# Kernel tuning notes

Hardware: AMD Instinct MI355X
Metric: run time of the kernel (lower is better)

## Reference

```python
import jax, jax.numpy as jnp
import numpy as np
import math

B, L, C, H = 8, 1024, 1024, 8
EPS = 1e-5

def setup_inputs() -> dict:
    key = jax.random.key(0)
    ks = jax.random.split(key, 5)
    s = 0.02
    return {
        "x": jax.random.normal(ks[0], (B, L, C), dtype=jnp.float32),
        "ln_g": jnp.ones((C,), dtype=jnp.float32),
        "ln_b": jnp.zeros((C,), dtype=jnp.float32),
        "w_qkv": jax.random.normal(ks[1], (C, 3 * C), dtype=jnp.float32) * s,
        "b_qkv": jax.random.normal(ks[2], (3 * C,), dtype=jnp.float32) * s,
        "w_out": jax.random.normal(ks[3], (C, C), dtype=jnp.float32) * s,
        "b_out": jax.random.normal(ks[4], (C,), dtype=jnp.float32) * s,
    }

def reference(x, ln_g, ln_b, w_qkv, b_qkv, w_out, b_out):
    bs, length, width = x.shape
    ch = width // H
    # LayerNorm over channels
    mu = jnp.mean(x, axis=-1, keepdims=True)
    var = jnp.mean(jnp.square(x - mu), axis=-1, keepdims=True)
    xn = (x - mu) * jax.lax.rsqrt(var + EPS) * ln_g + ln_b
    # fused QKV projection
    qkv = jnp.einsum('blc,cd->bld', xn, w_qkv) + b_qkv  # [B, L, 3C]
    q, k, v = jnp.split(qkv, 3, axis=2)                 # each [B, L, C]
    scale = 1.0 / math.sqrt(math.sqrt(ch))
    # faithful raw row-major reshape as in the torch .view call
    q = (q * scale).reshape(bs * H, length, ch)
    k = (k * scale).reshape(bs * H, length, ch)
    v = v.reshape(bs * H, length, ch)
    w = jnp.einsum('bqc,bkc->bqk', q, k)                # [B*H, L, L] score matrix
    w = jax.nn.softmax(w.astype(jnp.float32), axis=-1).astype(q.dtype)
    attn = jnp.einsum('bqk,bkc->bqc', w, v).reshape(bs, length, -1)
    out = jnp.einsum('blc,cd->bld', attn, w_out) + b_out + xn  # residual uses normalized x
    return out
```

## Files before the change

kernel.cpp:

```cpp
#include <hip/hip_runtime.h>
#include <hip/hip_bf16.h>


typedef __attribute__((ext_vector_type(8))) short short8;
typedef __attribute__((ext_vector_type(4))) float f32x4;

#define QK_SCALE 0.29730177875068026f

__device__ __forceinline__ float bf2f(ushort u) {
    union { float f; unsigned int i; } c; c.i = ((unsigned int)u) << 16; return c.f;
}
__device__ __forceinline__ ushort f2bf(float f) {
    union { float f; unsigned int i; } c; c.f = f;
    unsigned int x = c.i;
    return (ushort)((x + 0x7FFFu + ((x >> 16) & 1u)) >> 16);
}

__device__ __forceinline__ void gload_lds16(const ushort* g, ushort* l) {
    __builtin_amdgcn_global_load_lds(
        (const __attribute__((address_space(1))) unsigned int*)g,
        (__attribute__((address_space(3))) unsigned int*)l, 16, 0, 0);
}

__global__ __launch_bounds__(256) void ln_kernel(
    const float* __restrict__ x, const float* __restrict__ g,
    const float* __restrict__ b, ushort* __restrict__ xn) {
    int row = blockIdx.x;
    int tid = threadIdx.x;
    const float* xr = x + (size_t)row * 1024;
    float4 v4 = *(const float4*)(xr + tid * 4);
    float v[4] = {v4.x, v4.y, v4.z, v4.w};
    float s1 = 0.f, s2 = 0.f;
#pragma unroll
    for (int j = 0; j < 4; j++) { s1 += v[j]; s2 += v[j] * v[j]; }
#pragma unroll
    for (int m = 32; m >= 1; m >>= 1) { s1 += __shfl_xor(s1, m); s2 += __shfl_xor(s2, m); }
    __shared__ float r1[4], r2[4];
    int lane = tid & 63, w = tid >> 6;
    if (lane == 0) { r1[w] = s1; r2[w] = s2; }
    __syncthreads();
    s1 = r1[0] + r1[1] + r1[2] + r1[3];
    s2 = r2[0] + r2[1] + r2[2] + r2[3];
    float mu = s1 * (1.0f / 1024.0f);
    float var = s2 * (1.0f / 1024.0f) - mu * mu;
    float rs = rsqrtf(var + 1e-5f);
    int c0 = tid * 4;
    float4 gg = *(const float4*)(g + c0);
    float4 bb = *(const float4*)(b + c0);
    float gA[4] = {gg.x, gg.y, gg.z, gg.w};
    float bA[4] = {bb.x, bb.y, bb.z, bb.w};
    ushort o[4];
#pragma unroll
    for (int j = 0; j < 4; j++) o[j] = f2bf((v[j] - mu) * rs * gA[j] + bA[j]);
    uint2 pk;
    pk.x = (uint)o[0] | ((uint)o[1] << 16);
    pk.y = (uint)o[2] | ((uint)o[3] << 16);
    *(uint2*)(xn + (size_t)row * 1024 + c0) = pk;
}

__global__ __launch_bounds__(256) void transpose_kernel(
    const float* __restrict__ in, ushort* __restrict__ out, int R, int Cc) {
    __shared__ ushort t[32][33];
    int bx = blockIdx.x * 32, by = blockIdx.y * 32;
    int tx = threadIdx.x & 31, ty = threadIdx.x >> 5;
#pragma unroll
    for (int j = 0; j < 32; j += 8)
        t[ty + j][tx] = f2bf(in[(size_t)(by + ty + j) * Cc + bx + tx]);
    __syncthreads();
#pragma unroll
    for (int j = 0; j < 32; j += 8)
        out[(size_t)(bx + ty + j) * R + by + tx] = t[tx][ty + j];
}

__global__ __launch_bounds__(256) void transpose_head(
    const ushort* __restrict__ in, ushort* __restrict__ out) {
    __shared__ ushort t[32][33];
    int h = blockIdx.z;
    int j0 = blockIdx.y * 32;
    int d0 = blockIdx.x * 32;
    int tx = threadIdx.x & 31, ty = threadIdx.x >> 5;
    const ushort* src = in + (size_t)h * 131072;
    ushort* dst = out + (size_t)h * 131072;
#pragma unroll
    for (int j = 0; j < 32; j += 8)
        t[ty + j][tx] = src[(size_t)(j0 + ty + j) * 128 + d0 + tx];
    __syncthreads();
#pragma unroll
    for (int j = 0; j < 32; j += 8)
        dst[(size_t)(d0 + ty + j) * 1024 + j0 + tx] = t[tx][ty + j];
}

__global__ __launch_bounds__(256) void gemm_qkv(
    const ushort* __restrict__ A, const ushort* __restrict__ Bt,
    const float* __restrict__ bias, ushort* __restrict__ out0,
    ushort* __restrict__ out1, ushort* __restrict__ out2) {
    const int K = 1024;
    __shared__ __align__(16) ushort As[128 * 64];
    __shared__ __align__(16) ushort Bs[128 * 64];

    int tid = threadIdx.x;
    int lane = tid & 63, w = tid >> 6;
    int l15 = lane & 15, q4 = lane >> 4;
    int wr = (w >> 1) * 64, wc = (w & 1) * 64;
    int rowBase = blockIdx.y * 128, colBase = blockIdx.x * 128;

    f32x4 acc[4][4];
    f32x4 zero = {0.f, 0.f, 0.f, 0.f};
#pragma unroll
    for (int mi = 0; mi < 4; mi++)
#pragma unroll
        for (int ni = 0; ni < 4; ni++) acc[mi][ni] = zero;

    for (int kt = 0; kt < 16; kt++) {
        __syncthreads();
#pragma unroll
        for (int i = 0; i < 4; i++) {
            int linear = i * 256 + w * 64 + lane;
            int r = linear >> 3, p = linear & 7;
            int l = p ^ (r & 7);
            gload_lds16(&A[(size_t)(rowBase + r) * K + kt * 64 + l * 8], &As[linear * 8]);
            gload_lds16(&Bt[(size_t)(colBase + r) * K + kt * 64 + l * 8], &Bs[linear * 8]);
        }
        __syncthreads();

#pragma unroll
        for (int kk = 0; kk < 2; kk++) {
            short8 aF[4], bF[4];
#pragma unroll
            for (int mi = 0; mi < 4; mi++) {
                int r = wr + mi * 16 + l15;
                aF[mi] = *(const short8*)&As[r * 64 + ((kk * 4 + q4) ^ (r & 7)) * 8];
            }
#pragma unroll
            for (int ni = 0; ni < 4; ni++) {
                int r = wc + ni * 16 + l15;
                bF[ni] = *(const short8*)&Bs[r * 64 + ((kk * 4 + q4) ^ (r & 7)) * 8];
            }
#pragma unroll
            for (int mi = 0; mi < 4; mi++)
#pragma unroll
                for (int ni = 0; ni < 4; ni++)
                    acc[mi][ni] = __builtin_amdgcn_mfma_f32_16x16x32_bf16(
                        aF[mi], bF[ni], acc[mi][ni], 0, 0, 0);
        }
    }

#pragma unroll
    for (int mi = 0; mi < 4; mi++)
#pragma unroll
        for (int ni = 0; ni < 4; ni++) {
            f32x4 a = acc[mi][ni];
            int col = colBase + wc + ni * 16 + l15;
            float bv = bias[col];
#pragma unroll
            for (int r = 0; r < 4; r++) {
                int row = rowBase + wr + mi * 16 + q4 * 4 + r;
                float val = a[r] + bv;
                if (col < 2048) val *= QK_SCALE;
                int bsel = col >> 10, cc = col & 1023;
                ushort* dst = (bsel == 0) ? out0 : ((bsel == 1) ? out1 : out2);
                dst[(size_t)row * 1024 + cc] = f2bf(val);
            }
        }
}

__global__ __launch_bounds__(256, 4) void gemm_out(
    const ushort* __restrict__ A, const ushort* __restrict__ Bt,
    const float* __restrict__ bias, const ushort* __restrict__ resid,
    float* __restrict__ outf) {
    const int K = 1024;
    __shared__ __align__(16) ushort As[64 * 64];
    __shared__ __align__(16) ushort Bs[128 * 64];

    int tid = threadIdx.x;
    int lane = tid & 63, w = tid >> 6;
    int l15 = lane & 15, q4 = lane >> 4;
    int wr = (w >> 1) * 32, wc = (w & 1) * 64;
    int rowBase = blockIdx.y * 64, colBase = blockIdx.x * 128;

    f32x4 acc[2][4];
    f32x4 zero = {0.f, 0.f, 0.f, 0.f};
#pragma unroll
    for (int mi = 0; mi < 2; mi++)
#pragma unroll
        for (int ni = 0; ni < 4; ni++) acc[mi][ni] = zero;

    for (int kt = 0; kt < 16; kt++) {
        __syncthreads();
#pragma unroll
        for (int i = 0; i < 6; i++) {
            int id = i * 256 + w * 64 + lane;
            if (id < 512) {
                int r = id >> 3, p = id & 7;
                int l = p ^ (r & 7);
                gload_lds16(&A[(size_t)(rowBase + r) * K + kt * 64 + l * 8], &As[id * 8]);
            } else {
                int idb = id - 512;
                int r = idb >> 3, p = idb & 7;
                int l = p ^ (r & 7);
                gload_lds16(&Bt[(size_t)(colBase + r) * K + kt * 64 + l * 8], &Bs[idb * 8]);
            }
        }
        __syncthreads();

#pragma unroll
        for (int kk = 0; kk < 2; kk++) {
            short8 aF[2], bF[4];
#pragma unroll
            for (int mi = 0; mi < 2; mi++) {
                int r = wr + mi * 16 + l15;
                aF[mi] = *(const short8*)&As[r * 64 + ((kk * 4 + q4) ^ (r & 7)) * 8];
            }
#pragma unroll
            for (int ni = 0; ni < 4; ni++) {
                int r = wc + ni * 16 + l15;
                bF[ni] = *(const short8*)&Bs[r * 64 + ((kk * 4 + q4) ^ (r & 7)) * 8];
            }
#pragma unroll
            for (int mi = 0; mi < 2; mi++)
#pragma unroll
                for (int ni = 0; ni < 4; ni++)
                    acc[mi][ni] = __builtin_amdgcn_mfma_f32_16x16x32_bf16(
                        aF[mi], bF[ni], acc[mi][ni], 0, 0, 0);
        }
    }

#pragma unroll
    for (int mi = 0; mi < 2; mi++)
#pragma unroll
        for (int ni = 0; ni < 4; ni++) {
            f32x4 a = acc[mi][ni];
            int col = colBase + wc + ni * 16 + l15;
            float bv = bias[col];
#pragma unroll
            for (int r = 0; r < 4; r++) {
                int row = rowBase + wr + mi * 16 + q4 * 4 + r;
                float val = a[r] + bv + bf2f(resid[(size_t)row * 1024 + col]);
                outf[(size_t)row * 1024 + col] = val;
            }
        }
}

__global__ __launch_bounds__(256, 4) void attn_kernel(
    const ushort* __restrict__ qb, const ushort* __restrict__ kb,
    const ushort* __restrict__ vt, ushort* __restrict__ ob) {
    int g = blockIdx.x >> 4;
    int qblk = blockIdx.x & 15;
    const ushort* Qh = qb + (size_t)g * 131072;
    const ushort* Kh = kb + (size_t)g * 131072;
    const ushort* Vh = vt + (size_t)g * 131072;

    __shared__ __align__(16) ushort Ks[64 * 128];
    __shared__ __align__(16) ushort Vt[128 * 64];
    __shared__ __align__(16) ushort Ps[64 * 64];

    int tid = threadIdx.x, lane = tid & 63, w = tid >> 6;
    int l15 = lane & 15, q4 = lane >> 4;
    int q0 = qblk * 64;

    short8 qf[4];
#pragma unroll
    for (int ks = 0; ks < 4; ks++)
        qf[ks] = *(const short8*)&Qh[(size_t)(q0 + w * 16 + l15) * 128 + ks * 32 + q4 * 8];

    f32x4 zero = {0.f, 0.f, 0.f, 0.f};
    f32x4 o[8];
#pragma unroll
    for (int ni = 0; ni < 8; ni++) o[ni] = zero;
    float plsum[4] = {0.f, 0.f, 0.f, 0.f};

    for (int kt = 0; kt < 16; kt++) {
        __syncthreads();
#pragma unroll
        for (int i = 0; i < 4; i++) {
            int linear = i * 256 + w * 64 + lane;
            int r = linear >> 4, p = linear & 15;
            int l = p ^ (r & 15);
            gload_lds16(&Kh[(size_t)(kt * 64 + r) * 128 + l * 8], &Ks[linear * 8]);
        }
#pragma unroll
        for (int i = 0; i < 4; i++) {
            int id = i * 256 + tid;
            int d = id >> 3, c = id & 7;
            int pc = c ^ (d & 7);
            *(uint4*)&Vt[d * 64 + pc * 8] =
                *(const uint4*)&Vh[(size_t)d * 1024 + kt * 64 + c * 8];
        }
        __syncthreads();

        f32x4 sacc[4];
#pragma unroll
        for (int ni = 0; ni < 4; ni++) sacc[ni] = zero;
#pragma unroll
        for (int ks = 0; ks < 4; ks++) {
#pragma unroll
            for (int ni = 0; ni < 4; ni++) {
                int r = ni * 16 + l15;
                int p = (ks * 4 + q4) ^ (r & 15);
                short8 bF = *(const short8*)&Ks[r * 128 + p * 8];
                sacc[ni] = __builtin_amdgcn_mfma_f32_16x16x32_bf16(
                    qf[ks], bF, sacc[ni], 0, 0, 0);
            }
        }

#pragma unroll
        for (int ni = 0; ni < 4; ni++) {
#pragma unroll
            for (int r = 0; r < 4; r++) {
                float pv = __expf(sacc[ni][r]);
                plsum[r] += pv;
                int qloc = w * 16 + q4 * 4 + r;
                int key = ni * 16 + l15;
                int pc = (key >> 3) ^ (qloc & 7);
                Ps[qloc * 64 + pc * 8 + (key & 7)] = f2bf(pv);
            }
        }

#pragma unroll
        for (int ks2 = 0; ks2 < 2; ks2++) {
            int c = ks2 * 4 + q4;
            short8 aF = *(const short8*)&Ps[(w * 16 + l15) * 64 + (c ^ (l15 & 7)) * 8];
#pragma unroll
            for (int ni = 0; ni < 8; ni++) {
                int d = ni * 16 + l15;
                short8 bF = *(const short8*)&Vt[d * 64 + (c ^ (d & 7)) * 8];
                o[ni] = __builtin_amdgcn_mfma_f32_16x16x32_bf16(aF, bF, o[ni], 0, 0, 0);
            }
        }
    }

#pragma unroll
    for (int r = 0; r < 4; r++) {
#pragma unroll
        for (int m = 1; m < 16; m <<= 1) plsum[r] += __shfl_xor(plsum[r], m, 16);
    }
    float inv[4];
#pragma unroll
    for (int r = 0; r < 4; r++) inv[r] = 1.0f / plsum[r];
#pragma unroll
    for (int ni = 0; ni < 8; ni++)
#pragma unroll
        for (int r = 0; r < 4; r++) {
            int qrow = q0 + w * 16 + q4 * 4 + r;
            ob[(size_t)g * 131072 + (size_t)qrow * 128 + ni * 16 + l15] =
                f2bf(o[ni][r] * inv[r]);
        }
}

extern "C" void kernel_launch(void* const* d_in, const int* in_sizes, int n_in,
                              void* d_out, int out_size, void* d_ws, size_t ws_size,
                              hipStream_t stream) {
    const float* x     = (const float*)d_in[0];
    const float* ln_g  = (const float*)d_in[1];
    const float* ln_b  = (const float*)d_in[2];
    const float* w_qkv = (const float*)d_in[3];
    const float* b_qkv = (const float*)d_in[4];
    const float* w_out = (const float*)d_in[5];
    const float* b_out = (const float*)d_in[6];
    float* out = (float*)d_out;

    const size_t MC = 8192ull * 1024ull;
    ushort* xn    = (ushort*)d_ws;
    ushort* wqkvT = xn + MC;
    ushort* woutT = wqkvT + 3072ull * 1024ull;
    ushort* qbuf  = woutT + 1024ull * 1024ull;
    ushort* kbuf  = qbuf + MC;
    ushort* vtbuf = kbuf + MC;
    ushort* attnb = vtbuf + MC;

    ln_kernel<<<8192, 256, 0, stream>>>(x, ln_g, ln_b, xn);
    transpose_kernel<<<dim3(96, 32), 256, 0, stream>>>(w_qkv, wqkvT, 1024, 3072);
    transpose_kernel<<<dim3(32, 32), 256, 0, stream>>>(w_out, woutT, 1024, 1024);
    gemm_qkv<<<dim3(24, 64), 256, 0, stream>>>(xn, wqkvT, b_qkv, qbuf, kbuf, attnb);
    transpose_head<<<dim3(4, 32, 64), 256, 0, stream>>>(attnb, vtbuf);
    attn_kernel<<<1024, 256, 0, stream>>>(qbuf, kbuf, vtbuf, attnb);
    gemm_out<<<dim3(8, 128), 256, 0, stream>>>(attnb, woutT, b_out, xn, out);
}
```

Before: 268.4 us.

## Merge prep kernels and write transposed V directly from QKV GEMM epilogue

LayerNorm and both weight transposes are merged into one prep kernel, with LayerNorm now handling one row per wavefront. The QKV GEMM epilogue writes V straight into the per-head transposed layout, so the separate transpose_head kernel and its extra round trip through global memory are gone. GEMM load addresses are precomputed and advanced by pointer increments rather than recomputed every k-step. The cost is strided, uncoalesced 2-byte stores in the V epilogue.

```diff
diff --git a/kernel.cpp b/kernel.cpp
--- a/kernel.cpp
+++ b/kernel.cpp
@@ -22,78 +22,73 @@
         (__attribute__((address_space(3))) unsigned int*)l, 16, 0, 0);
 }
 
-__global__ __launch_bounds__(256) void ln_kernel(
+__global__ __launch_bounds__(256) void prep_kernel(
     const float* __restrict__ x, const float* __restrict__ g,
-    const float* __restrict__ b, ushort* __restrict__ xn) {
-    int row = blockIdx.x;
+    const float* __restrict__ b, ushort* __restrict__ xn,
+    const float* __restrict__ w_qkv, ushort* __restrict__ wqkvT,
+    const float* __restrict__ w_out, ushort* __restrict__ woutT) {
+    __shared__ ushort t[32][33];
+    int bid = blockIdx.x;
     int tid = threadIdx.x;
-    const float* xr = x + (size_t)row * 1024;
-    float4 v4 = *(const float4*)(xr + tid * 4);
-    float v[4] = {v4.x, v4.y, v4.z, v4.w};
-    float s1 = 0.f, s2 = 0.f;
-#pragma unroll
-    for (int j = 0; j < 4; j++) { s1 += v[j]; s2 += v[j] * v[j]; }
-#pragma unroll
-    for (int m = 32; m >= 1; m >>= 1) { s1 += __shfl_xor(s1, m); s2 += __shfl_xor(s2, m); }
-    __shared__ float r1[4], r2[4];
-    int lane = tid & 63, w = tid >> 6;
-    if (lane == 0) { r1[w] = s1; r2[w] = s2; }
-    __syncthreads();
-    s1 = r1[0] + r1[1] + r1[2] + r1[3];
-    s2 = r2[0] + r2[1] + r2[2] + r2[3];
-    float mu = s1 * (1.0f / 1024.0f);
-    float var = s2 * (1.0f / 1024.0f) - mu * mu;
-    float rs = rsqrtf(var + 1e-5f);
-    int c0 = tid * 4;
-    float4 gg = *(const float4*)(g + c0);
-    float4 bb = *(const float4*)(b + c0);
-    float gA[4] = {gg.x, gg.y, gg.z, gg.w};
-    float bA[4] = {bb.x, bb.y, bb.z, bb.w};
-    ushort o[4];
-#pragma unroll
-    for (int j = 0; j < 4; j++) o[j] = f2bf((v[j] - mu) * rs * gA[j] + bA[j]);
-    uint2 pk;
-    pk.x = (uint)o[0] | ((uint)o[1] << 16);
-    pk.y = (uint)o[2] | ((uint)o[3] << 16);
-    *(uint2*)(xn + (size_t)row * 1024 + c0) = pk;
-}
-
-__global__ __launch_bounds__(256) void transpose_kernel(
-    const float* __restrict__ in, ushort* __restrict__ out, int R, int Cc) {
-    __shared__ ushort t[32][33];
-    int bx = blockIdx.x * 32, by = blockIdx.y * 32;
-    int tx = threadIdx.x & 31, ty = threadIdx.x >> 5;
-#pragma unroll
-    for (int j = 0; j < 32; j += 8)
-        t[ty + j][tx] = f2bf(in[(size_t)(by + ty + j) * Cc + bx + tx]);
-    __syncthreads();
-#pragma unroll
-    for (int j = 0; j < 32; j += 8)
-        out[(size_t)(bx + ty + j) * R + by + tx] = t[tx][ty + j];
-}
-
-__global__ __launch_bounds__(256) void transpose_head(
-    const ushort* __restrict__ in, ushort* __restrict__ out) {
-    __shared__ ushort t[32][33];
-    int h = blockIdx.z;
-    int j0 = blockIdx.y * 32;
-    int d0 = blockIdx.x * 32;
-    int tx = threadIdx.x & 31, ty = threadIdx.x >> 5;
-    const ushort* src = in + (size_t)h * 131072;
-    ushort* dst = out + (size_t)h * 131072;
-#pragma unroll
-    for (int j = 0; j < 32; j += 8)
-        t[ty + j][tx] = src[(size_t)(j0 + ty + j) * 128 + d0 + tx];
-    __syncthreads();
-#pragma unroll
-    for (int j = 0; j < 32; j += 8)
-        dst[(size_t)(d0 + ty + j) * 1024 + j0 + tx] = t[tx][ty + j];
+    if (bid < 2048) {
+        int w = tid >> 6, lane = tid & 63;
+        int row = bid * 4 + w;
+        const float* xr = x + (size_t)row * 1024;
+        float v[4][4];
+        float s1 = 0.f, s2 = 0.f;
+#pragma unroll
+        for (int j = 0; j < 4; j++) {
+            float4 t4 = *(const float4*)(xr + lane * 4 + j * 256);
+            v[j][0] = t4.x; v[j][1] = t4.y; v[j][2] = t4.z; v[j][3] = t4.w;
+#pragma unroll
+            for (int e = 0; e < 4; e++) { s1 += v[j][e]; s2 += v[j][e] * v[j][e]; }
+        }
+#pragma unroll
+        for (int m = 32; m >= 1; m >>= 1) { s1 += __shfl_xor(s1, m); s2 += __shfl_xor(s2, m); }
+        float mu = s1 * (1.0f / 1024.0f);
+        float var = s2 * (1.0f / 1024.0f) - mu * mu;
+        float rs = rsqrtf(var + 1e-5f);
+#pragma unroll
+        for (int j = 0; j < 4; j++) {
+            int c0 = lane * 4 + j * 256;
+            float4 gg = *(const float4*)(g + c0);
+            float4 bb = *(const float4*)(b + c0);
+            float gA[4] = {gg.x, gg.y, gg.z, gg.w};
+            float bA[4] = {bb.x, bb.y, bb.z, bb.w};
+            ushort o[4];
+#pragma unroll
+            for (int e = 0; e < 4; e++) o[e] = f2bf((v[j][e] - mu) * rs * gA[e] + bA[e]);
+            uint2 pk;
+            pk.x = (uint)o[0] | ((uint)o[1] << 16);
+            pk.y = (uint)o[2] | ((uint)o[3] << 16);
+            *(uint2*)(xn + (size_t)row * 1024 + c0) = pk;
+        }
+    } else {
+        const float* in; ushort* out; int R, Cc, bx, by;
+        if (bid < 5120) {
+            int tt = bid - 2048;
+            in = w_qkv; out = wqkvT; R = 1024; Cc = 3072;
+            bx = (tt % 96) * 32; by = (tt / 96) * 32;
+        } else {
+            int tt = bid - 5120;
+            in = w_out; out = woutT; R = 1024; Cc = 1024;
+            bx = (tt % 32) * 32; by = (tt / 32) * 32;
+        }
+        int tx = tid & 31, ty = tid >> 5;
+#pragma unroll
+        for (int j = 0; j < 32; j += 8)
+            t[ty + j][tx] = f2bf(in[(size_t)(by + ty + j) * Cc + bx + tx]);
+        __syncthreads();
+#pragma unroll
+        for (int j = 0; j < 32; j += 8)
+            out[(size_t)(bx + ty + j) * R + by + tx] = t[tx][ty + j];
+    }
 }
 
 __global__ __launch_bounds__(256) void gemm_qkv(
     const ushort* __restrict__ A, const ushort* __restrict__ Bt,
     const float* __restrict__ bias, ushort* __restrict__ out0,
-    ushort* __restrict__ out1, ushort* __restrict__ out2) {
+    ushort* __restrict__ out1, ushort* __restrict__ vtb) {
     const int K = 1024;
     __shared__ __align__(16) ushort As[128 * 64];
     __shared__ __align__(16) ushort Bs[128 * 64];
@@ -104,6 +99,19 @@
     int wr = (w >> 1) * 64, wc = (w & 1) * 64;
     int rowBase = blockIdx.y * 128, colBase = blockIdx.x * 128;
 
+    const ushort* aS[4]; const ushort* bS[4];
+    ushort* aD[4]; ushort* bD[4];
+#pragma unroll
+    for (int i = 0; i < 4; i++) {
+        int linear = i * 256 + w * 64 + lane;
+        int r = linear >> 3;
+        int l = (linear & 7) ^ (r & 7);
+        aS[i] = A + (size_t)(rowBase + r) * K + l * 8;
+        bS[i] = Bt + (size_t)(colBase + r) * K + l * 8;
+        aD[i] = &As[linear * 8];
+        bD[i] = &Bs[linear * 8];
+    }
+
     f32x4 acc[4][4];
     f32x4 zero = {0.f, 0.f, 0.f, 0.f};
 #pragma unroll
@@ -115,11 +123,9 @@
         __syncthreads();
 #pragma unroll
         for (int i = 0; i < 4; i++) {
-            int linear = i * 256 + w * 64 + lane;
-            int r = linear >> 3, p = linear & 7;
-            int l = p ^ (r & 7);
-            gload_lds16(&A[(size_t)(rowBase + r) * K + kt * 64 + l * 8], &As[linear * 8]);
-            gload_lds16(&Bt[(size_t)(colBase + r) * K + kt * 64 + l * 8], &Bs[linear * 8]);
+            gload_lds16(aS[i], aD[i]);
+            gload_lds16(bS[i], bD[i]);
+            aS[i] += 64; bS[i] += 64;
         }
         __syncthreads();
 
@@ -146,22 +152,35 @@
     }
 
 #pragma unroll
-    for (int mi = 0; mi < 4; mi++)
-#pragma unroll
-        for (int ni = 0; ni < 4; ni++) {
-            f32x4 a = acc[mi][ni];
-            int col = colBase + wc + ni * 16 + l15;
-            float bv = bias[col];
-#pragma unroll
-            for (int r = 0; r < 4; r++) {
-                int row = rowBase + wr + mi * 16 + q4 * 4 + r;
-                float val = a[r] + bv;
-                if (col < 2048) val *= QK_SCALE;
-                int bsel = col >> 10, cc = col & 1023;
-                ushort* dst = (bsel == 0) ? out0 : ((bsel == 1) ? out1 : out2);
-                dst[(size_t)row * 1024 + cc] = f2bf(val);
-            }
-        }
+    for (int ni = 0; ni < 4; ni++) {
+        int col = colBase + wc + ni * 16 + l15;
+        float bv = bias[col];
+        int bsel = col >> 10, cc = col & 1023;
+        if (bsel == 2) {
+            ushort* dst = vtb + (size_t)blockIdx.y * 131072
+                          + (size_t)(cc & 127) * 1024 + (cc >> 7);
+#pragma unroll
+            for (int mi = 0; mi < 4; mi++) {
+                f32x4 a = acc[mi][ni];
+#pragma unroll
+                for (int r = 0; r < 4; r++) {
+                    int rl = wr + mi * 16 + q4 * 4 + r;
+                    dst[rl * 8] = f2bf(a[r] + bv);
+                }
+            }
+        } else {
+            ushort* dst = (bsel == 0) ? out0 : out1;
+#pragma unroll
+            for (int mi = 0; mi < 4; mi++) {
+                f32x4 a = acc[mi][ni];
+#pragma unroll
+                for (int r = 0; r < 4; r++) {
+                    int row = rowBase + wr + mi * 16 + q4 * 4 + r;
+                    dst[(size_t)row * 1024 + cc] = f2bf((a[r] + bv) * QK_SCALE);
+                }
+            }
+        }
+    }
 }
 
 __global__ __launch_bounds__(256, 4) void gemm_out(
@@ -178,6 +197,22 @@
     int wr = (w >> 1) * 32, wc = (w & 1) * 64;
     int rowBase = blockIdx.y * 64, colBase = blockIdx.x * 128;
 
+    const ushort* src[6]; ushort* dstp[6];
+#pragma unroll
+    for (int i = 0; i < 6; i++) {
+        int id = i * 256 + w * 64 + lane;
+        if (id < 512) {
+            int r = id >> 3, l = (id & 7) ^ ((id >> 3) & 7);
+            src[i] = A + (size_t)(rowBase + r) * K + l * 8;
+            dstp[i] = &As[id * 8];
+        } else {
+            int idb = id - 512;
+            int r = idb >> 3, l = (idb & 7) ^ ((idb >> 3) & 7);
+            src[i] = Bt + (size_t)(colBase + r) * K + l * 8;
+            dstp[i] = &Bs[idb * 8];
+        }
+    }
+
     f32x4 acc[2][4];
     f32x4 zero = {0.f, 0.f, 0.f, 0.f};
 #pragma unroll
@@ -189,17 +224,8 @@
         __syncthreads();
 #pragma unroll
         for (int i = 0; i < 6; i++) {
-            int id = i * 256 + w * 64 + lane;
-            if (id < 512) {
-                int r = id >> 3, p = id & 7;
-                int l = p ^ (r & 7);
-                gload_lds16(&A[(size_t)(rowBase + r) * K + kt * 64 + l * 8], &As[id * 8]);
-            } else {
-                int idb = id - 512;
-                int r = idb >> 3, p = idb & 7;
-                int l = p ^ (r & 7);
-                gload_lds16(&Bt[(size_t)(colBase + r) * K + kt * 64 + l * 8], &Bs[idb * 8]);
-            }
+            gload_lds16(src[i], dstp[i]);
+            src[i] += 64;
         }
         __syncthreads();
 
@@ -226,19 +252,20 @@
     }
 
 #pragma unroll
-    for (int mi = 0; mi < 2; mi++)
-#pragma unroll
-        for (int ni = 0; ni < 4; ni++) {
+    for (int ni = 0; ni < 4; ni++) {
+        int col = colBase + wc + ni * 16 + l15;
+        float bv = bias[col];
+#pragma unroll
+        for (int mi = 0; mi < 2; mi++) {
             f32x4 a = acc[mi][ni];
-            int col = colBase + wc + ni * 16 + l15;
-            float bv = bias[col];
 #pragma unroll
             for (int r = 0; r < 4; r++) {
                 int row = rowBase + wr + mi * 16 + q4 * 4 + r;
-                float val = a[r] + bv + bf2f(resid[(size_t)row * 1024 + col]);
-                outf[(size_t)row * 1024 + col] = val;
-            }
-        }
+                outf[(size_t)row * 1024 + col] =
+                    a[r] + bv + bf2f(resid[(size_t)row * 1024 + col]);
+            }
+        }
+    }
 }
 
 __global__ __launch_bounds__(256, 4) void attn_kernel(
@@ -368,11 +395,8 @@
     ushort* vtbuf = kbuf + MC;
     ushort* attnb = vtbuf + MC;
 
-    ln_kernel<<<8192, 256, 0, stream>>>(x, ln_g, ln_b, xn);
-    transpose_kernel<<<dim3(96, 32), 256, 0, stream>>>(w_qkv, wqkvT, 1024, 3072);
-    transpose_kernel<<<dim3(32, 32), 256, 0, stream>>>(w_out, woutT, 1024, 1024);
-    gemm_qkv<<<dim3(24, 64), 256, 0, stream>>>(xn, wqkvT, b_qkv, qbuf, kbuf, attnb);
-    transpose_head<<<dim3(4, 32, 64), 256, 0, stream>>>(attnb, vtbuf);
+    prep_kernel<<<6144, 256, 0, stream>>>(x, ln_g, ln_b, xn, w_qkv, wqkvT, w_out, woutT);
+    gemm_qkv<<<dim3(24, 64), 256, 0, stream>>>(xn, wqkvT, b_qkv, qbuf, kbuf, vtbuf);
     attn_kernel<<<1024, 256, 0, stream>>>(qbuf, kbuf, vtbuf, attnb);
     gemm_out<<<dim3(8, 128), 256, 0, stream>>>(attnb, woutT, b_out, xn, out);
 }
```

Result: slower. 303.0 us (+12.9%).
